# Kernel optimization log

Hardware: AMD Instinct MI355X
Metric: run time of the kernel (lower is better)

The kernel has to match this reference:

```python
import jax, jax.numpy as jnp
import numpy as np

S = 2048      # sequence length
E = 2048      # n_embd
H = 16        # n_head
D = E // H    # head_dim = 128
EPS = 1e-5


def _layer_norm(x, w):
    # eqx.nn.LayerNorm, use_bias=False: (x - mean) / sqrt(var + eps) * w
    mu = jnp.mean(x, axis=-1, keepdims=True)
    var = jnp.mean(jnp.square(x - mu), axis=-1, keepdims=True)
    return (x - mu) * jax.lax.rsqrt(var + EPS) * w


def setup_inputs() -> dict:
    key = jax.random.key(0)
    ks = jax.random.split(key, 7)
    x = jax.random.normal(ks[0], (S, E), dtype=jnp.float32)
    # equinox Linear weights are (out_features, in_features); y = W @ x
    w_attn = jax.random.normal(ks[1], (3 * E, E), dtype=jnp.float32) * 0.02
    w_proj_attn = jax.random.normal(ks[2], (E, E), dtype=jnp.float32) * 0.02
    w_fc = jax.random.normal(ks[3], (4 * E, E), dtype=jnp.float32) * 0.02
    w_proj_ffn = jax.random.normal(ks[4], (E, 4 * E), dtype=jnp.float32) * 0.02
    ln1_w = jnp.ones((E,), dtype=jnp.float32)
    ln2_w = jnp.ones((E,), dtype=jnp.float32)
    return {"x": x, "ln1_w": ln1_w, "ln2_w": ln2_w, "w_attn": w_attn,
            "w_proj_attn": w_proj_attn, "w_fc": w_fc, "w_proj_ffn": w_proj_ffn}


def reference(x, ln1_w, ln2_w, w_attn, w_proj_attn, w_fc, w_proj_ffn):
    # --- LN1 + fused QKV projection ---
    h = _layer_norm(x, ln1_w)                       # [S, E]
    qkv = h @ w_attn.T                              # [S, 3E]
    q, k, v = jnp.split(qkv, 3, axis=-1)
    q = q.reshape(S, H, D)
    k = k.reshape(S, H, D)
    v = v.reshape(S, H, D)
    # --- naive causal attention with materialized [H, S, T] scores ---
    scale = 1.0 / jnp.sqrt(jnp.float32(D))
    causal_bias = (jnp.arange(S)[:, None] < jnp.arange(S)[None, :]) * (-10000.0)
    scores = jnp.einsum('shd,thd->hst', q, k) * scale + causal_bias  # [H,S,T]
    probs = jax.nn.softmax(scores, axis=-1)
    attn = jnp.einsum('hst,thd->shd', probs, v).reshape(S, E)
    x = x + attn @ w_proj_attn.T
    # --- LN2 + GELU MLP ---
    h2 = _layer_norm(x, ln2_w)                      # [S, E]
    f = jax.nn.gelu(h2 @ w_fc.T) @ w_proj_ffn.T    # [S,4E] -> [S,E]
    return x + f
```

## Files before the change

kernel.cpp:

```cpp
#include <hip/hip_runtime.h>
#include <hip/hip_bf16.h>

#define S_LEN 2048
#define EMB   2048
#define NH    16
#define HD    128

typedef __bf16 bf16x8 __attribute__((ext_vector_type(8)));
typedef __bf16 bf16x4 __attribute__((ext_vector_type(4)));
typedef float  f32x4  __attribute__((ext_vector_type(4)));
typedef short  s16x4  __attribute__((ext_vector_type(4)));

__device__ __forceinline__ void async_copy16(void* lds, const void* g) {
  __builtin_amdgcn_global_load_lds((__attribute__((address_space(1))) void*)(void*)g,
                                   (__attribute__((address_space(3))) void*)lds, 16, 0, 0);
}

__device__ __forceinline__ unsigned lds_addr(const void* p) {
  return (unsigned)(uintptr_t)(const __attribute__((address_space(3))) char*)p;
}

__device__ __forceinline__ s16x4 tr16(unsigned addr) {
  s16x4 d;
  asm volatile("ds_read_b64_tr_b16 %0, %1" : "=v"(d) : "v"(addr));
  return d;
}

__device__ __forceinline__ float gelu_tanh(float x) {
  float x3 = x * x * x;
  float t  = 0.7978845608028654f * (x + 0.044715f * x3);
  float th = 1.0f - 2.0f / (__expf(2.0f * t) + 1.0f);
  return 0.5f * x * (1.0f + th);
}

__global__ __launch_bounds__(256) void prologue_kernel(const float* __restrict__ s0,
                                                       const float* __restrict__ s1,
                                                       const float* __restrict__ s2,
                                                       const float* __restrict__ s3,
                                                       __bf16* __restrict__ d0,
                                                       __bf16* __restrict__ d1,
                                                       __bf16* __restrict__ d2,
                                                       __bf16* __restrict__ d3,
                                                       const float* __restrict__ x,
                                                       const float* __restrict__ lnw,
                                                       __bf16* __restrict__ lnout) {
  const int t = threadIdx.x;
  if (blockIdx.x < 49152) {
    size_t i = ((size_t)blockIdx.x * 256 + t) * 4;
    const float* s; __bf16* d; size_t off;
    if (i < 12582912ull)       { s = s0; d = d0; off = i; }
    else if (i < 16777216ull)  { s = s1; d = d1; off = i - 12582912ull; }
    else if (i < 33554432ull)  { s = s2; d = d2; off = i - 16777216ull; }
    else                       { s = s3; d = d3; off = i - 33554432ull; }
    float4 v = *(const float4*)(s + off);
    bf16x4 o;
    o[0] = (__bf16)v.x; o[1] = (__bf16)v.y; o[2] = (__bf16)v.z; o[3] = (__bf16)v.w;
    *(bf16x4*)(d + off) = o;
    return;
  }
  int row = blockIdx.x - 49152;
  const float* xr = x + (size_t)row * EMB;
  float4 a = *(const float4*)(xr + t * 8);
  float4 b = *(const float4*)(xr + t * 8 + 4);
  float s  = a.x + a.y + a.z + a.w + b.x + b.y + b.z + b.w;
  float sq = a.x*a.x + a.y*a.y + a.z*a.z + a.w*a.w + b.x*b.x + b.y*b.y + b.z*b.z + b.w*b.w;
  #pragma unroll
  for (int o = 32; o > 0; o >>= 1) { s += __shfl_xor(s, o); sq += __shfl_xor(sq, o); }
  __shared__ float red[8];
  if ((t & 63) == 0) { red[t >> 6] = s; red[(t >> 6) + 4] = sq; }
  __syncthreads();
  s  = red[0] + red[1] + red[2] + red[3];
  sq = red[4] + red[5] + red[6] + red[7];
  float mu  = s * (1.0f / EMB);
  float var = sq * (1.0f / EMB) - mu * mu;
  float rs  = rsqrtf(var + 1e-5f);
  float4 w1 = *(const float4*)(lnw + t * 8);
  float4 w2 = *(const float4*)(lnw + t * 8 + 4);
  bf16x8 ov;
  ov[0] = (__bf16)((a.x - mu) * rs * w1.x);
  ov[1] = (__bf16)((a.y - mu) * rs * w1.y);
  ov[2] = (__bf16)((a.z - mu) * rs * w1.z);
  ov[3] = (__bf16)((a.w - mu) * rs * w1.w);
  ov[4] = (__bf16)((b.x - mu) * rs * w2.x);
  ov[5] = (__bf16)((b.y - mu) * rs * w2.y);
  ov[6] = (__bf16)((b.z - mu) * rs * w2.z);
  ov[7] = (__bf16)((b.w - mu) * rs * w2.w);
  *(bf16x8*)(lnout + (size_t)row * EMB + t * 8) = ov;
}

__global__ __launch_bounds__(256) void ln_fuse_kernel(const float* __restrict__ x,
                                                      const __bf16* __restrict__ part,
                                                      const float* __restrict__ w,
                                                      __bf16* __restrict__ hout,
                                                      float* __restrict__ resout) {
  int row = blockIdx.x;
  int t = threadIdx.x;
  const size_t base = (size_t)row * EMB + t * 8;
  float r[8];
  {
    float4 a = *(const float4*)(x + base);
    float4 b = *(const float4*)(x + base + 4);
    r[0] = a.x; r[1] = a.y; r[2] = a.z; r[3] = a.w;
    r[4] = b.x; r[5] = b.y; r[6] = b.z; r[7] = b.w;
    #pragma unroll
    for (int z = 0; z < 4; z++) {
      bf16x8 p = *(const bf16x8*)(part + (size_t)z * S_LEN * EMB + base);
      #pragma unroll
      for (int k = 0; k < 8; k++) r[k] += (float)p[k];
    }
  }
  float s = 0.f, sq = 0.f;
  #pragma unroll
  for (int k = 0; k < 8; k++) { s += r[k]; sq += r[k] * r[k]; }
  #pragma unroll
  for (int o = 32; o > 0; o >>= 1) { s += __shfl_xor(s, o); sq += __shfl_xor(sq, o); }
  __shared__ float red[8];
  if ((t & 63) == 0) { red[t >> 6] = s; red[(t >> 6) + 4] = sq; }
  __syncthreads();
  s  = red[0] + red[1] + red[2] + red[3];
  sq = red[4] + red[5] + red[6] + red[7];
  float mu  = s * (1.0f / EMB);
  float var = sq * (1.0f / EMB) - mu * mu;
  float rs  = rsqrtf(var + 1e-5f);
  float4 w1 = *(const float4*)(w + t * 8);
  float4 w2 = *(const float4*)(w + t * 8 + 4);
  float wv[8] = {w1.x, w1.y, w1.z, w1.w, w2.x, w2.y, w2.z, w2.w};
  bf16x8 ov;
  #pragma unroll
  for (int k = 0; k < 8; k++) ov[k] = (__bf16)((r[k] - mu) * rs * wv[k]);
  *(bf16x8*)(hout + base) = ov;
  float4 o1 = make_float4(r[0], r[1], r[2], r[3]);
  float4 o2 = make_float4(r[4], r[5], r[6], r[7]);
  *(float4*)(resout + base) = o1;
  *(float4*)(resout + base + 4) = o2;
}

__global__ __launch_bounds__(256) void add4_kernel(float* __restrict__ out,
                                                   const __bf16* __restrict__ part) {
  size_t i = ((size_t)blockIdx.x * 256 + threadIdx.x) * 4;
  float4 o = *(const float4*)(out + i);
  #pragma unroll
  for (int z = 0; z < 4; z++) {
    bf16x4 p = *(const bf16x4*)(part + (size_t)z * S_LEN * EMB + i);
    o.x += (float)p[0]; o.y += (float)p[1]; o.z += (float)p[2]; o.w += (float)p[3];
  }
  *(float4*)(out + i) = o;
}

#define MFMA16(AV, BV, MG)                                                                   \
  _Pragma("unroll")                                                                          \
  for (int m = 0; m < 4; m++)                                                                \
    _Pragma("unroll")                                                                        \
    for (int n = 0; n < 4; n++)                                                              \
      acc[(MG) * 4 + m][n] =                                                                 \
          __builtin_amdgcn_mfma_f32_16x16x32_bf16(AV[m], BV[n], acc[(MG) * 4 + m][n], 0, 0, 0);

#define PHASE_TOP()                                                                          \
  __builtin_amdgcn_s_barrier();                                                              \
  __builtin_amdgcn_s_setprio(1);

#define PHASE_BOT()                                                                          \
  __builtin_amdgcn_s_setprio(0);                                                             \
  __builtin_amdgcn_s_barrier();

template <int EPI>
__global__ __launch_bounds__(512, 2) void gemm256(const __bf16* __restrict__ A,
                                                  const __bf16* __restrict__ B,
                                                  void* __restrict__ Cv,
                                                  int M, int N, int K, int Ksl,
                                                  int NN, int NSPLIT) {
  __shared__ __bf16 As[2 * 2 * 256 * 32];
  __shared__ __bf16 Bs[2 * 2 * 256 * 32];

  const int t = threadIdx.x, w = t >> 6, l = t & 63;
  const int fr = l & 15, g = l >> 4;
  const int wr = w >> 2, wc = w & 3;

  const int nwg = gridDim.x;
  const int wg = (blockIdx.x & 7) * (nwg >> 3) + (blockIdx.x >> 3);
  const int z = wg % NSPLIT;
  const int tile = wg / NSPLIT;
  const int my = tile / NN, nx = tile - my * NN;
  const int m0 = my * 256, n0 = nx * 256;
  const int kb = z * Ksl;
  const int NT = Ksl >> 6;

  const int srow = t >> 2;
  const int schunk = (t & 3) ^ ((t >> 3) & 3);
  const __bf16* Abase = A + (size_t)(m0 + srow) * K + kb + schunk * 8;
  const __bf16* Bbase = B + (size_t)(n0 + srow) * K + kb + schunk * 8;
  const size_t K128 = (size_t)128 * K;
  __bf16* AsT = &As[t * 8];
  __bf16* BsT = &Bs[t * 8];

  auto stage = [&](const __bf16* base, __bf16* dstT, int kt, int kh) {
    const __bf16* src = base + kt * 64 + kh * 32;
    __bf16* dst = dstT + ((kt & 1) * 2 + kh) * 8192;
    async_copy16(dst, src);
    async_copy16(dst + 4096, src + K128);
  };

  const int gran = (g ^ ((fr >> 1) & 3)) << 3;
  auto rdA = [&](bf16x8* dst, int kt, int kh, int mg) {
    const int ub = ((kt & 1) * 2 + kh) * 256;
    #pragma unroll
    for (int m = 0; m < 4; m++) {
      int row = wr * 128 + (mg * 4 + m) * 16 + fr;
      dst[m] = *(const bf16x8*)&As[(ub + row) * 32 + gran];
    }
  };
  auto rdB = [&](bf16x8* dst, int kt, int kh) {
    const int ub = ((kt & 1) * 2 + kh) * 256;
    #pragma unroll
    for (int n = 0; n < 4; n++) {
      int row = wc * 64 + n * 16 + fr;
      dst[n] = *(const bf16x8*)&Bs[(ub + row) * 32 + gran];
    }
  };

  f32x4 acc[8][4] = {};
  bf16x8 av[4], bX[4], bY[4];

  stage(Abase, AsT, 0, 0); stage(Bbase, BsT, 0, 0);
  stage(Abase, AsT, 0, 1); stage(Bbase, BsT, 0, 1);
  if (NT > 1) { stage(Abase, AsT, 1, 0); stage(Bbase, BsT, 1, 0); }
  asm volatile("s_waitcnt vmcnt(4)" ::: "memory");
  __builtin_amdgcn_s_barrier();

  for (int kt = 0; kt < NT; ++kt) {
    const bool s1 = (kt + 1 < NT), s2 = (kt + 2 < NT);
    rdB(bX, kt, 0);
    rdA(av, kt, 0, 0);
    if (s1) stage(Abase, AsT, kt + 1, 1);
    PHASE_TOP();
    MFMA16(av, bX, 0);
    PHASE_BOT();
    rdA(av, kt, 0, 1);
    if (s1) stage(Bbase, BsT, kt + 1, 1);
    PHASE_TOP();
    MFMA16(av, bX, 1);
    __builtin_amdgcn_s_setprio(0);
    if (s1) { asm volatile("s_waitcnt vmcnt(4)" ::: "memory"); }
    else    { asm volatile("s_waitcnt vmcnt(0)" ::: "memory"); }
    __builtin_amdgcn_s_barrier();
    rdB(bY, kt, 1);
    rdA(av, kt, 1, 0);
    if (s2) stage(Abase, AsT, kt + 2, 0);
    PHASE_TOP();
    MFMA16(av, bY, 0);
    PHASE_BOT();
    rdA(av, kt, 1, 1);
    if (s2) stage(Bbase, BsT, kt + 2, 0);
    PHASE_TOP();
    MFMA16(av, bY, 1);
    PHASE_BOT();
  }

  const size_t zoff = (size_t)z * M * N;
  #pragma unroll
  for (int m = 0; m < 8; m++)
    #pragma unroll
    for (int n = 0; n < 4; n++)
      #pragma unroll
      for (int j = 0; j < 4; j++) {
        int orow = m0 + wr * 128 + m * 16 + g * 4 + j;
        int ocol = n0 + wc * 64 + n * 16 + fr;
        size_t idx = (size_t)orow * N + ocol;
        float v = acc[m][n][j];
        if (EPI == 0) {
          ((__bf16*)Cv)[idx] = (__bf16)v;
        } else if (EPI == 2) {
          ((__bf16*)Cv)[idx] = (__bf16)gelu_tanh(v);
        } else {
          ((__bf16*)Cv)[zoff + idx] = (__bf16)v;
        }
      }
}

template <int EPI>
__global__ __launch_bounds__(512, 4) void gemm128(const __bf16* __restrict__ A,
                                                  const __bf16* __restrict__ B,
                                                  void* __restrict__ Cv,
                                                  int M, int N, int K, int Ksl,
                                                  int NN, int NSPLIT) {
  __shared__ __bf16 As[3][128 * 32];
  __shared__ __bf16 Bs[3][256 * 32];

  const int t = threadIdx.x, w = t >> 6, l = t & 63;
  const int fr = l & 15, g = l >> 4;
  const int wr = w >> 2, wc = w & 3;

  const int nwg = gridDim.x;
  const int wg = (blockIdx.x & 7) * (nwg >> 3) + (blockIdx.x >> 3);
  const int z = wg % NSPLIT;
  const int tile = wg / NSPLIT;
  const int my = tile / NN, nx = tile - my * NN;
  const int m0 = my * 128, n0 = nx * 256;
  const int kb = z * Ksl;
  const int NT = Ksl >> 5;

  const int srow = t >> 2;
  const int schunk = (t & 3) ^ ((t >> 3) & 3);
  const __bf16* Abase = A + (size_t)(m0 + srow) * K + kb + schunk * 8;
  const __bf16* Bbase = B + (size_t)(n0 + srow) * K + kb + schunk * 8;
  const size_t K128 = (size_t)128 * K;

  auto stage = [&](int kt, int slot) {
    const __bf16* sa = Abase + kt * 32;
    const __bf16* sb = Bbase + kt * 32;
    async_copy16(&As[slot][t * 8], sa);
    async_copy16(&Bs[slot][t * 8], sb);
    async_copy16(&Bs[slot][t * 8 + 4096], sb + K128);
  };

  const int gran = (g ^ ((fr >> 1) & 3)) << 3;

  f32x4 acc[4][4] = {};

  stage(0, 0);
  stage(1, 1);
  asm volatile("s_waitcnt vmcnt(3)" ::: "memory");
  __builtin_amdgcn_s_barrier();

  int sc = 0, s1 = 1, s2 = 2;
  for (int kt = 0; kt < NT; ++kt) {
    bf16x8 a[4], b[4];
    #pragma unroll
    for (int m = 0; m < 4; m++)
      a[m] = *(const bf16x8*)&As[sc][(wr * 64 + m * 16 + fr) * 32 + gran];
    #pragma unroll
    for (int n = 0; n < 4; n++)
      b[n] = *(const bf16x8*)&Bs[sc][(wc * 64 + n * 16 + fr) * 32 + gran];
    if (kt + 2 < NT) stage(kt + 2, s2);
    __builtin_amdgcn_s_setprio(1);
    #pragma unroll
    for (int m = 0; m < 4; m++)
      #pragma unroll
      for (int n = 0; n < 4; n++)
        acc[m][n] = __builtin_amdgcn_mfma_f32_16x16x32_bf16(a[m], b[n], acc[m][n], 0, 0, 0);
    __builtin_amdgcn_s_setprio(0);
    if (kt + 1 < NT) {
      if (kt + 2 < NT) { asm volatile("s_waitcnt vmcnt(3)" ::: "memory"); }
      else             { asm volatile("s_waitcnt vmcnt(0)" ::: "memory"); }
    }
    __builtin_amdgcn_s_barrier();
    int tmp = sc; sc = s1; s1 = s2; s2 = tmp;
  }

  const size_t zoff = (size_t)z * M * N;
  #pragma unroll
  for (int m = 0; m < 4; m++)
    #pragma unroll
    for (int n = 0; n < 4; n++)
      #pragma unroll
      for (int j = 0; j < 4; j++) {
        int orow = m0 + wr * 64 + m * 16 + g * 4 + j;
        int ocol = n0 + wc * 64 + n * 16 + fr;
        size_t idx = (size_t)orow * N + ocol;
        float v = acc[m][n][j];
        if (EPI == 0) {
          ((__bf16*)Cv)[idx] = (__bf16)v;
        } else if (EPI == 2) {
          ((__bf16*)Cv)[idx] = (__bf16)gelu_tanh(v);
        } else {
          ((__bf16*)Cv)[zoff + idx] = (__bf16)v;
        }
      }
}

__global__ __launch_bounds__(512, 2) void attn_kernel(const __bf16* __restrict__ qkv,
                                                      __bf16* __restrict__ out) {
  __shared__ __bf16 Kt[2][64 * 128];
  __shared__ __bf16 Vt[2][64 * 128];
  __shared__ __bf16 Pb[8][16 * 64];

  const int bid = blockIdx.x;
  const int h = bid & 15;
  const int pi = bid >> 4;
  const int qbA = pi, qbB = 31 - pi;

  const int t = threadIdx.x, w = t >> 6, l = t & 63;
  const int g = l >> 4, fr = l & 15;
  const int fkb = g * 8;
  const int myqb = (w < 4) ? qbA : qbB;
  const int q0 = myqb * 64 + (w & 3) * 16;
  const float scale = 0.08838834764831845f;

  const int kchunk = fr ^ ((w * 4 + g) & 7);
  const int vkey = (l >> 1) & 3;
  const int vd0  = (l >> 3) * 16 + (l & 1) * 8;

  const size_t row3E = (size_t)(3 * EMB);
  const __bf16* Kg = qkv + EMB + h * HD;
  const __bf16* Vg = qkv + 2 * EMB + h * HD;

  bf16x8 qf[4];
  #pragma unroll
  for (int kc = 0; kc < 4; kc++)
    qf[kc] = *(const bf16x8*)&qkv[(size_t)(q0 + fr) * row3E + h * HD + kc * 32 + fkb];

  f32x4 o[8] = {};
  float mrun[4] = {-1e30f, -1e30f, -1e30f, -1e30f};
  float lsum[4] = {0.f, 0.f, 0.f, 0.f};

  const unsigned vtrb[2] = { lds_addr(&Vt[0][0]) + g * 2048 + fr * 8,
                             lds_addr(&Vt[1][0]) + g * 2048 + fr * 8 };

  auto stage = [&](int buf, int it) {
    const int t0 = it * 64;
    #pragma unroll
    for (int r = 0; r < 2; r++) {
      async_copy16(&Kt[buf][(r * 8 + w) * 512],
                   Kg + (size_t)(t0 + (r * 8 + w) * 4 + g) * row3E + kchunk * 8);
      async_copy16(&Vt[buf][(r * 8 + w) * 512],
                   Vg + (size_t)(t0 + (r * 8 + w) * 4 + vkey) * row3E + vd0);
    }
  };

  const int nt = qbB + 1;
  stage(0, 0);
  int cur = 0;

  for (int it = 0; it < nt; it++) {
    __syncthreads();
    if (it + 1 < nt) stage(cur ^ 1, it + 1);

    if (it <= myqb) {
      const int t0 = it * 64;
      f32x4 s[4] = {};
      __builtin_amdgcn_s_setprio(1);
      #pragma unroll
      for (int n = 0; n < 4; n++)
        #pragma unroll
        for (int kc = 0; kc < 4; kc++) {
          bf16x8 kf = *(const bf16x8*)&Kt[cur][(n * 16 + fr) * 128 +
                                              (((kc * 4 + g) ^ (fr & 7)) << 3)];
          s[n] = __builtin_amdgcn_mfma_f32_16x16x32_bf16(qf[kc], kf, s[n], 0, 0, 0);
        }
      __builtin_amdgcn_s_setprio(0);
      #pragma unroll
      for (int n = 0; n < 4; n++)
        #pragma unroll
        for (int j = 0; j < 4; j++) {
          int tcol = t0 + n * 16 + fr;
          int qrow = q0 + g * 4 + j;
          float v = s[n][j] * scale;
          s[n][j] = (tcol > qrow) ? -1e30f : v;
        }
      float pm[4];
      #pragma unroll
      for (int j = 0; j < 4; j++) {
        pm[j] = fmaxf(fmaxf(s[0][j], s[1][j]), fmaxf(s[2][j], s[3][j]));
        #pragma unroll
        for (int off = 1; off < 16; off <<= 1) pm[j] = fmaxf(pm[j], __shfl_xor(pm[j], off));
      }
      float factor[4];
      #pragma unroll
      for (int j = 0; j < 4; j++) {
        float mn = fmaxf(mrun[j], pm[j]);
        factor[j] = __expf(mrun[j] - mn);
        mrun[j] = mn;
      }
      float rs[4] = {0.f, 0.f, 0.f, 0.f};
      #pragma unroll
      for (int n = 0; n < 4; n++)
        #pragma unroll
        for (int j = 0; j < 4; j++) {
          float p = __expf(s[n][j] - mrun[j]);
          s[n][j] = p;
          rs[j] += p;
        }
      #pragma unroll
      for (int j = 0; j < 4; j++) {
        #pragma unroll
        for (int off = 1; off < 16; off <<= 1) rs[j] += __shfl_xor(rs[j], off);
        lsum[j] = lsum[j] * factor[j] + rs[j];
      }
      #pragma unroll
      for (int b = 0; b < 8; b++)
        #pragma unroll
        for (int j = 0; j < 4; j++) o[b][j] *= factor[j];

      #pragma unroll
      for (int n = 0; n < 4; n++)
        #pragma unroll
        for (int j = 0; j < 4; j++) {
          int q   = g * 4 + j;
          int key = n * 16 + fr;
          int cs  = (key >> 3) ^ (q & 7);
          Pb[w][q * 64 + cs * 8 + (key & 7)] = (__bf16)s[n][j];
        }

      bf16x8 pf[2];
      #pragma unroll
      for (int kc = 0; kc < 2; kc++)
        pf[kc] = *(const bf16x8*)&Pb[w][fr * 64 + (((kc * 4 + g) ^ (fr & 7)) << 3)];

      const unsigned vtr = vtrb[cur];
      __builtin_amdgcn_s_setprio(1);
      #pragma unroll
      for (int b = 0; b < 8; b++) {
        s16x4 t00 = tr16(vtr + b * 128);
        s16x4 t01 = tr16(vtr + b * 128 + 1024);
        s16x4 t10 = tr16(vtr + b * 128 + 8192);
        s16x4 t11 = tr16(vtr + b * 128 + 8192 + 1024);
        asm volatile("s_waitcnt lgkmcnt(0)");
        __builtin_amdgcn_sched_barrier(0);
        union { s16x4 hh[2]; bf16x8 v; } u0, u1;
        u0.hh[0] = t00; u0.hh[1] = t01;
        u1.hh[0] = t10; u1.hh[1] = t11;
        o[b] = __builtin_amdgcn_mfma_f32_16x16x32_bf16(pf[0], u0.v, o[b], 0, 0, 0);
        o[b] = __builtin_amdgcn_mfma_f32_16x16x32_bf16(pf[1], u1.v, o[b], 0, 0, 0);
      }
      __builtin_amdgcn_s_setprio(0);
    }
    cur ^= 1;
  }

  float rcp[4];
  #pragma unroll
  for (int j = 0; j < 4; j++) rcp[j] = 1.0f / lsum[j];
  #pragma unroll
  for (int b = 0; b < 8; b++)
    #pragma unroll
    for (int j = 0; j < 4; j++) {
      int qrow = q0 + g * 4 + j;
      out[(size_t)qrow * EMB + h * HD + b * 16 + fr] = (__bf16)(o[b][j] * rcp[j]);
    }
}

extern "C" void kernel_launch(void* const* d_in, const int* in_sizes, int n_in,
                              void* d_out, int out_size, void* d_ws, size_t ws_size,
                              hipStream_t stream) {
  const float* x     = (const float*)d_in[0];
  const float* ln1w  = (const float*)d_in[1];
  const float* ln2w  = (const float*)d_in[2];
  const float* wattn = (const float*)d_in[3];
  const float* wproja= (const float*)d_in[4];
  const float* wfc   = (const float*)d_in[5];
  const float* wprojf= (const float*)d_in[6];
  float* out = (float*)d_out;
  char* ws = (char*)d_ws;

  __bf16* wattn_b  = (__bf16*)(ws);
  __bf16* wproja_b = (__bf16*)(ws + 25165824);
  __bf16* wfc_b    = (__bf16*)(ws + 33554432);
  __bf16* wprojf_b = (__bf16*)(ws + 67108864);
  __bf16* h_b      = (__bf16*)(ws + 100663296);
  __bf16* qkv_b    = (__bf16*)(ws + 109051904);
  __bf16* attn_b   = (__bf16*)(ws + 134217728);
  __bf16* f1_b     = (__bf16*)(ws + 142606336);
  __bf16* p1_part  = f1_b;
  __bf16* p2_part  = qkv_b;

  prologue_kernel<<<51200, 256, 0, stream>>>(wattn, wproja, wfc, wprojf,
                                             wattn_b, wproja_b, wfc_b, wprojf_b,
                                             x, ln1w, h_b);
  gemm256<0><<<192, 512, 0, stream>>>(h_b, wattn_b, qkv_b, S_LEN, 3 * EMB, EMB, EMB, 24, 1);
  attn_kernel<<<dim3(256), 512, 0, stream>>>(qkv_b, attn_b);
  gemm128<5><<<512, 512, 0, stream>>>(attn_b, wproja_b, p1_part, S_LEN, EMB, EMB, EMB / 4, 8, 4);
  ln_fuse_kernel<<<S_LEN, 256, 0, stream>>>(x, p1_part, ln2w, h_b, out);
  gemm256<2><<<256, 512, 0, stream>>>(h_b, wfc_b, f1_b, S_LEN, 4 * EMB, EMB, EMB, 32, 1);
  gemm256<5><<<256, 512, 0, stream>>>(f1_b, wprojf_b, p2_part, S_LEN, EMB, 4 * EMB, 2048, 8, 4);
  add4_kernel<<<4096, 256, 0, stream>>>(out, p2_part);
}
```

Before: 395.3 us.

## Overlap remaining weight casts with attention kernel via extra blocks

Result: no change. 396.5 us (+0.3%).

```diff
diff --git a/kernel.cpp b/kernel.cpp
--- a/kernel.cpp
+++ b/kernel.cpp
@@ -34,31 +34,20 @@
 }
 
 __global__ __launch_bounds__(256) void prologue_kernel(const float* __restrict__ s0,
-                                                       const float* __restrict__ s1,
-                                                       const float* __restrict__ s2,
-                                                       const float* __restrict__ s3,
                                                        __bf16* __restrict__ d0,
-                                                       __bf16* __restrict__ d1,
-                                                       __bf16* __restrict__ d2,
-                                                       __bf16* __restrict__ d3,
                                                        const float* __restrict__ x,
                                                        const float* __restrict__ lnw,
                                                        __bf16* __restrict__ lnout) {
   const int t = threadIdx.x;
-  if (blockIdx.x < 49152) {
+  if (blockIdx.x < 12288) {
     size_t i = ((size_t)blockIdx.x * 256 + t) * 4;
-    const float* s; __bf16* d; size_t off;
-    if (i < 12582912ull)       { s = s0; d = d0; off = i; }
-    else if (i < 16777216ull)  { s = s1; d = d1; off = i - 12582912ull; }
-    else if (i < 33554432ull)  { s = s2; d = d2; off = i - 16777216ull; }
-    else                       { s = s3; d = d3; off = i - 33554432ull; }
-    float4 v = *(const float4*)(s + off);
+    float4 v = *(const float4*)(s0 + i);
     bf16x4 o;
     o[0] = (__bf16)v.x; o[1] = (__bf16)v.y; o[2] = (__bf16)v.z; o[3] = (__bf16)v.w;
-    *(bf16x4*)(d + off) = o;
+    *(bf16x4*)(d0 + i) = o;
     return;
   }
-  int row = blockIdx.x - 49152;
+  int row = blockIdx.x - 12288;
   const float* xr = x + (size_t)row * EMB;
   float4 a = *(const float4*)(xr + t * 8);
   float4 b = *(const float4*)(xr + t * 8 + 4);
@@ -369,17 +358,37 @@
 }
 
 __global__ __launch_bounds__(512, 2) void attn_kernel(const __bf16* __restrict__ qkv,
-                                                      __bf16* __restrict__ out) {
+                                                      __bf16* __restrict__ out,
+                                                      const float* __restrict__ c1,
+                                                      const float* __restrict__ c2,
+                                                      const float* __restrict__ c3,
+                                                      __bf16* __restrict__ e1,
+                                                      __bf16* __restrict__ e2,
+                                                      __bf16* __restrict__ e3) {
   __shared__ __bf16 Kt[2][64 * 128];
   __shared__ __bf16 Vt[2][64 * 128];
   __shared__ __bf16 Pb[8][16 * 64];
+
+  const int t = threadIdx.x, w = t >> 6, l = t & 63;
+
+  if (blockIdx.x >= 256) {
+    size_t i = ((size_t)(blockIdx.x - 256) * 512 + t) * 4;
+    const float* s; __bf16* d; size_t off;
+    if (i < 4194304ull)        { s = c1; d = e1; off = i; }
+    else if (i < 20971520ull)  { s = c2; d = e2; off = i - 4194304ull; }
+    else                       { s = c3; d = e3; off = i - 20971520ull; }
+    float4 v = *(const float4*)(s + off);
+    bf16x4 o;
+    o[0] = (__bf16)v.x; o[1] = (__bf16)v.y; o[2] = (__bf16)v.z; o[3] = (__bf16)v.w;
+    *(bf16x4*)(d + off) = o;
+    return;
+  }
 
   const int bid = blockIdx.x;
   const int h = bid & 15;
   const int pi = bid >> 4;
   const int qbA = pi, qbB = 31 - pi;
 
-  const int t = threadIdx.x, w = t >> 6, l = t & 63;
   const int g = l >> 4, fr = l & 15;
   const int fkb = g * 8;
   const int myqb = (w < 4) ? qbA : qbB;
@@ -553,11 +562,11 @@
   __bf16* p1_part  = f1_b;
   __bf16* p2_part  = qkv_b;
 
-  prologue_kernel<<<51200, 256, 0, stream>>>(wattn, wproja, wfc, wprojf,
-                                             wattn_b, wproja_b, wfc_b, wprojf_b,
-                                             x, ln1w, h_b);
+  prologue_kernel<<<14336, 256, 0, stream>>>(wattn, wattn_b, x, ln1w, h_b);
   gemm256<0><<<192, 512, 0, stream>>>(h_b, wattn_b, qkv_b, S_LEN, 3 * EMB, EMB, EMB, 24, 1);
-  attn_kernel<<<dim3(256), 512, 0, stream>>>(qkv_b, attn_b);
+  attn_kernel<<<dim3(256 + 18432), 512, 0, stream>>>(qkv_b, attn_b,
+                                                     wproja, wfc, wprojf,
+                                                     wproja_b, wfc_b, wprojf_b);
   gemm128<5><<<512, 512, 0, stream>>>(attn_b, wproja_b, p1_part, S_LEN, EMB, EMB, EMB / 4, 8, 4);
   ln_fuse_kernel<<<S_LEN, 256, 0, stream>>>(x, p1_part, ln2w, h_b, out);
   gemm256<2><<<256, 512, 0, stream>>>(h_b, wfc_b, f1_b, S_LEN, 4 * EMB, EMB, EMB, 32, 1);
```
